# Kernel optimization log

Measured on AMD Instinct MI355X. Metric: run time of the kernel, lower is better.

The kernel has to match this reference:

```python
import jax, jax.numpy as jnp
import numpy as np

B, N, H = 32, 1024, 256
ALPHA = 0.2  # leaky relu slope
NEG_INF = -1e12


def setup_inputs() -> dict:
    key = jax.random.key(0)
    k1, k2, k3, k4, k5, k6 = jax.random.split(key, 6)
    inp = jax.random.normal(k1, (B, N, H), dtype=jnp.float32)
    A = (jax.random.uniform(k2, (B, N, N)) < 0.05).astype(jnp.float32)
    l = jnp.sort(jax.random.randint(k3, (B, 2), 0, N), axis=1)
    # xavier-uniform(gain=1.414) approximated; exact init values are irrelevant for correctness
    lim_w = 1.414 * np.sqrt(6.0 / (H + H))
    W_i = jax.random.uniform(k4, (H, H), minval=-lim_w, maxval=lim_w, dtype=jnp.float32)
    W_c = jax.random.uniform(k5, (H, H), minval=-lim_w, maxval=lim_w, dtype=jnp.float32)
    lim_a = 1.414 * np.sqrt(6.0 / (2 * H + 1))
    a = jax.random.uniform(k6, (2 * H, 1), minval=-lim_a, maxval=lim_a, dtype=jnp.float32)
    return {"inp": inp, "A": A, "l": l, "W_i": W_i, "W_c": W_c, "a": a}


def reference(inp, A, l, W_i, W_c, a):
    # eval mode: dropout is identity (training=False)
    n = inp.shape[1]
    h = inp.shape[2]
    Wh_i = jnp.einsum('bnh,he->bne', inp, W_i)
    Wh_c = jnp.einsum('bnh,he->bne', inp, W_c)
    # vectorized replacement of the per-batch Wh[index][i:j] = Wh_i[index][i:j] loop
    idx = jnp.arange(n)
    sel = (idx[None, :] >= l[:, 0:1]) & (idx[None, :] < l[:, 1:2])  # [B,N]
    Wh = jnp.where(sel[:, :, None], Wh_i, Wh_c)
    # additive attention scores
    Wh1 = Wh @ a[:h, :]  # [B,N,1]
    Wh2 = Wh @ a[h:, :]  # [B,N,1]
    A_ = A + jnp.eye(n, dtype=A.dtype)
    e = jax.nn.leaky_relu((Wh1 + jnp.swapaxes(Wh2, 1, 2)) * A_, ALPHA)
    att = jnp.where(A_ > 0, e, NEG_INF)
    att = jax.nn.softmax(att, axis=2)
    h_prime = jnp.einsum('bnm,bme->bne', att, Wh)
    return jax.nn.elu(h_prime)  # concat=True
```

## Files before the change

kernel.cpp:

```cpp
#include <hip/hip_runtime.h>
#include <hip/hip_bf16.h>
#include <stdint.h>

#define B_ 32
#define N_ 1024
#define H_ 256
#define PF_PITCH 520
#define GEMM_BLOCKS (B_ * 16)

typedef short bf16x8 __attribute__((ext_vector_type(8)));
typedef float floatx4 __attribute__((ext_vector_type(4)));

__device__ inline unsigned short f2bs(float x) {
    __hip_bfloat16 h = __float2bfloat16(x);
    return __builtin_bit_cast(unsigned short, h);
}

__global__ __launch_bounds__(256)
void k_pre(const float* __restrict__ Wi, const float* __restrict__ Wc,
           const float* __restrict__ a, float* __restrict__ U,
           unsigned short* __restrict__ WtFi, unsigned short* __restrict__ WtFc) {
    int bid = blockIdx.x;
    int t = threadIdx.x;
    if (bid < 32) {
        __shared__ float tile[64][65];
        int mat = bid >> 4;
        int tr = ((bid >> 2) & 3) * 64;
        int tc = (bid & 3) * 64;
        const float* W = mat ? Wc : Wi;
        unsigned short* WtF = mat ? WtFc : WtFi;
        int rr = t >> 2, c4 = (t & 3) * 16;
        const float* src = W + (size_t)(tr + rr) * H_ + tc + c4;
#pragma unroll
        for (int j = 0; j < 4; ++j) {
            float4 v = *reinterpret_cast<const float4*>(src + j * 4);
            tile[rr][c4 + 4 * j + 0] = v.x;
            tile[rr][c4 + 4 * j + 1] = v.y;
            tile[rr][c4 + 4 * j + 2] = v.z;
            tile[rr][c4 + 4 * j + 3] = v.w;
        }
        __syncthreads();
#pragma unroll
        for (int h = 0; h < 2; ++h) {
            int s = h * 256 + t;
            int ksl = s >> 8;
            int cl  = (s >> 6) & 3;
            int ll  = s & 63;
            int m16v = ll & 15, quadv = ll >> 4;
            int nloc = cl * 16 + m16v;
            int kb = ksl * 32 + quadv * 8;
            unsigned int pk[4];
#pragma unroll
            for (int jj = 0; jj < 4; ++jj) {
                unsigned short lo = f2bs(tile[kb + 2 * jj][nloc]);
                unsigned short hi = f2bs(tile[kb + 2 * jj + 1][nloc]);
                pk[jj] = (unsigned int)lo | ((unsigned int)hi << 16);
            }
            int ksg = (tr >> 5) + ksl;
            int cg  = (tc >> 4) + cl;
            *reinterpret_cast<uint4*>(WtF + ((size_t)(ksg * 16 + cg) * 64 + ll) * 8) =
                *reinterpret_cast<uint4*>(pk);
        }
    } else {
        int k = bid - 32;
        float wi = Wi[k * H_ + t];
        float wc = Wc[k * H_ + t];
        float a1 = a[t], a2 = a[H_ + t];
        float p0 = wi * a1, p1 = wc * a1, p2 = wi * a2, p3 = wc * a2;
        for (int off = 32; off; off >>= 1) {
            p0 += __shfl_xor(p0, off);
            p1 += __shfl_xor(p1, off);
            p2 += __shfl_xor(p2, off);
            p3 += __shfl_xor(p3, off);
        }
        __shared__ float red[4][4];
        int w = t >> 6;
        if ((t & 63) == 0) { red[w][0] = p0; red[w][1] = p1; red[w][2] = p2; red[w][3] = p3; }
        __syncthreads();
        if (t == 0) {
            U[0 * H_ + k] = red[0][0] + red[1][0] + red[2][0] + red[3][0];
            U[1 * H_ + k] = red[0][1] + red[1][1] + red[2][1] + red[3][1];
            U[2 * H_ + k] = red[0][2] + red[1][2] + red[2][2] + red[3][2];
            U[3 * H_ + k] = red[0][3] + red[1][3] + red[2][3] + red[3][3];
        }
    }
}

__global__ __launch_bounds__(256, 2)
void k_main(const float* __restrict__ inp, const int* __restrict__ l,
            const unsigned short* __restrict__ WtFi, const unsigned short* __restrict__ WtFc,
            unsigned short* __restrict__ WhF, const float* __restrict__ U,
            float* __restrict__ Wh1, float* __restrict__ Wh2,
            const float* __restrict__ A, unsigned int* __restrict__ M) {
    int bid = blockIdx.x;
    int t = threadIdx.x;
    int w = t >> 6;
    int lane = t & 63;
    if (bid >= GEMM_BLOCKS) {
        size_t row = bid - GEMM_BLOCKS;
        const float* Ar = A + row * N_ + w * 256 + lane * 4;
        float4 v = *reinterpret_cast<const float4*>(Ar);
        unsigned long long b0 = __ballot(v.x > 0.f);
        unsigned long long b1 = __ballot(v.y > 0.f);
        unsigned long long b2 = __ballot(v.z > 0.f);
        unsigned long long b3 = __ballot(v.w > 0.f);
        if (lane == 0) {
            unsigned int* Mp = M + (row * 4 + w) * 8;
            uint4 v0 = {(unsigned int)b0, (unsigned int)(b0 >> 32),
                        (unsigned int)b1, (unsigned int)(b1 >> 32)};
            uint4 v1 = {(unsigned int)b2, (unsigned int)(b2 >> 32),
                        (unsigned int)b3, (unsigned int)(b3 >> 32)};
            *reinterpret_cast<uint4*>(Mp) = v0;
            *reinterpret_cast<uint4*>(Mp + 4) = v1;
        }
        return;
    }

    __shared__ unsigned short bbuf[2][8192];
    int blk = bid;
    int b  = blk >> 4;
    int r0 = (blk & 15) * 64;
    int quad = lane >> 4, m16 = lane & 15;
    int rowb = r0 + w * 16;

    int l0 = l[2 * b], l1 = l[2 * b + 1];
    bool allI = (l0 <= r0) && (r0 + 64 <= l1);
    bool allC = (l1 <= r0) || (l0 >= r0 + 64);
    int npass = (allI || allC) ? 1 : 2;

    int row = rowb + m16;
    bool sel = (row >= l0) && (row < l1);
    const float* xrow = inp + ((size_t)(b * N_ + row)) * H_;
    const float* u1 = U + (sel ? 0 : H_);
    const float* u2 = U + 2 * H_ + (sel ? 0 : H_);

    float d1 = 0.f, d2 = 0.f;
#pragma unroll 2
    for (int ks = 0; ks < 8; ++ks) {
        const float4 xa = *reinterpret_cast<const float4*>(xrow + ks * 32 + quad * 8);
        const float4 xb = *reinterpret_cast<const float4*>(xrow + ks * 32 + quad * 8 + 4);
        const float4 ua = *reinterpret_cast<const float4*>(u1 + ks * 32 + quad * 8);
        const float4 ub = *reinterpret_cast<const float4*>(u1 + ks * 32 + quad * 8 + 4);
        const float4 va = *reinterpret_cast<const float4*>(u2 + ks * 32 + quad * 8);
        const float4 vb = *reinterpret_cast<const float4*>(u2 + ks * 32 + quad * 8 + 4);
        d1 += xa.x * ua.x + xa.y * ua.y + xa.z * ua.z + xa.w * ua.w
            + xb.x * ub.x + xb.y * ub.y + xb.z * ub.z + xb.w * ub.w;
        d2 += xa.x * va.x + xa.y * va.y + xa.z * va.z + xa.w * va.w
            + xb.x * vb.x + xb.y * vb.y + xb.z * vb.z + xb.w * vb.w;
    }
    d1 += __shfl_xor(d1, 16); d1 += __shfl_xor(d1, 32);
    d2 += __shfl_xor(d2, 16); d2 += __shfl_xor(d2, 32);
    if (quad == 0) {
        Wh1[b * N_ + rowb + m16] = d1;
        Wh2[b * N_ + rowb + m16] = d2;
    }

    unsigned short* fb = WhF + (size_t)b * (N_ * H_);
    int j0 = rowb + quad * 4;
    int ksO = j0 >> 5;
    int laneF = m16 + 16 * ((j0 & 31) >> 3);
    int jj0 = j0 & 7;

    for (int pass = 0; pass < npass; ++pass) {
        const unsigned short* gbase =
            (npass == 1) ? (allI ? WtFi : WtFc) : (pass == 0 ? WtFi : WtFc);

        floatx4 acc[16];
#pragma unroll
        for (int c = 0; c < 16; ++c) acc[c] = (floatx4){0.f, 0.f, 0.f, 0.f};

        {
            const unsigned short* s0 = gbase + (size_t)t * 32;
#pragma unroll
            for (int j = 0; j < 4; ++j)
                *reinterpret_cast<uint4*>(&bbuf[0][t * 32 + j * 8]) =
                    *reinterpret_cast<const uint4*>(s0 + j * 8);
        }
        for (int ks = 0; ks < 8; ++ks) {
            __syncthreads();
            uint4 v[4];
            if (ks < 7) {
                const unsigned short* sn = gbase + (size_t)(ks + 1) * 8192 + t * 32;
#pragma unroll
                for (int j = 0; j < 4; ++j)
                    v[j] = *reinterpret_cast<const uint4*>(sn + j * 8);
            }
            const float4 xa = *reinterpret_cast<const float4*>(xrow + ks * 32 + quad * 8);
            const float4 xb = *reinterpret_cast<const float4*>(xrow + ks * 32 + quad * 8 + 4);
            unsigned int pk0 = (unsigned int)f2bs(xa.x) | ((unsigned int)f2bs(xa.y) << 16);
            unsigned int pk1 = (unsigned int)f2bs(xa.z) | ((unsigned int)f2bs(xa.w) << 16);
            unsigned int pk2 = (unsigned int)f2bs(xb.x) | ((unsigned int)f2bs(xb.y) << 16);
            unsigned int pk3 = (unsigned int)f2bs(xb.z) | ((unsigned int)f2bs(xb.w) << 16);
            uint4 apk = {pk0, pk1, pk2, pk3};
            bf16x8 af = __builtin_bit_cast(bf16x8, apk);

            const unsigned short* bptr = &bbuf[ks & 1][lane * 8];
#pragma unroll
            for (int c = 0; c < 16; ++c) {
                bf16x8 bfr = *reinterpret_cast<const bf16x8*>(bptr + c * 512);
                acc[c] = __builtin_amdgcn_mfma_f32_16x16x32_bf16(af, bfr, acc[c], 0, 0, 0);
            }
            if (ks < 7) {
#pragma unroll
                for (int j = 0; j < 4; ++j)
                    *reinterpret_cast<uint4*>(&bbuf[(ks + 1) & 1][t * 32 + j * 8]) = v[j];
            }
        }
        __syncthreads();

#pragma unroll
        for (int c = 0; c < 16; ++c) {
            size_t base = ((size_t)((ksO * 16 + c) * 64) + laneF) * 8 + jj0;
            if (npass == 1) {
                unsigned int lo = (unsigned int)f2bs(acc[c][0]) | ((unsigned int)f2bs(acc[c][1]) << 16);
                unsigned int hi = (unsigned int)f2bs(acc[c][2]) | ((unsigned int)f2bs(acc[c][3]) << 16);
                uint2 v2 = {lo, hi};
                *reinterpret_cast<uint2*>(fb + base) = v2;
            } else {
                bool want[4]; bool all = true, none = true;
#pragma unroll
                for (int r = 0; r < 4; ++r) {
                    int j = j0 + r;
                    bool s2 = (j >= l0) && (j < l1);
                    want[r] = (pass == 0) ? s2 : !s2;
                    all = all && want[r]; none = none && !want[r];
                }
                if (all) {
                    unsigned int lo = (unsigned int)f2bs(acc[c][0]) | ((unsigned int)f2bs(acc[c][1]) << 16);
                    unsigned int hi = (unsigned int)f2bs(acc[c][2]) | ((unsigned int)f2bs(acc[c][3]) << 16);
                    uint2 v2 = {lo, hi};
                    *reinterpret_cast<uint2*>(fb + base) = v2;
                } else if (!none) {
#pragma unroll
                    for (int r = 0; r < 4; ++r)
                        if (want[r]) fb[base + r] = f2bs(acc[c][r]);
                }
            }
        }
    }
}

__global__ __launch_bounds__(256)
void k_attn(const unsigned int* __restrict__ Mask, const float* __restrict__ Wh1,
            const float* __restrict__ Wh2, const unsigned short* __restrict__ WhF,
            float* __restrict__ out) {
    __shared__ unsigned short pfrag[2][32 * PF_PITCH];
    __shared__ float rsum[2][16];
    int t = threadIdx.x, w = t >> 6, lane = t & 63;
    int bi = blockIdx.x;
    int b = (bi & 7) * 4 + (bi >> 8);
    int tile = (bi >> 3) & 31;
    int rowbase = tile * 32;

    const float* Wh2b = Wh2 + b * N_;
    float4 w2v[4];
#pragma unroll
    for (int ch = 0; ch < 4; ++ch)
        w2v[ch] = *reinterpret_cast<const float4*>(Wh2b + ch * 256 + lane * 4);

    int ksl = lane >> 3;
    int q2 = (lane >> 1) & 3;
    int jj0 = (lane & 1) * 4;
    int d  = lane >> 5;
    int lb = lane & 31;

#pragma unroll
    for (int tt = 0; tt < 2; ++tt) {
#pragma unroll
        for (int q = 0; q < 4; ++q) {
            int m = w * 4 + q;
            int i = rowbase + tt * 16 + m;
            float wh1 = Wh1[b * N_ + i];
            const uint2* Mrow = reinterpret_cast<const uint2*>(
                Mask + ((size_t)(b * N_ + i)) * 32);
            unsigned int wv[4][4];
#pragma unroll
            for (int ch = 0; ch < 4; ++ch)
#pragma unroll
                for (int c = 0; c < 4; ++c) {
                    uint2 u = Mrow[ch * 4 + c];
                    wv[ch][c] = d ? u.y : u.x;
                }
            int s = m + 16 * q2;
            int sw = s ^ ((s >> 3) & 7);
            int sls = sw * 8 + jj0;
            float rp = 0.f;
#pragma unroll
            for (int ch = 0; ch < 4; ++ch) {
                float aa[4];
#pragma unroll
                for (int c = 0; c < 4; ++c)
                    aa[c] = (float)((wv[ch][c] >> lb) & 1u);
                if ((i >> 2) == (ch * 64 + lane)) aa[i & 3] += 1.0f;
                float ww[4] = {w2v[ch].x, w2v[ch].y, w2v[ch].z, w2v[ch].w};
                float p[4];
#pragma unroll
                for (int c = 0; c < 4; ++c) {
                    float e  = (wh1 + ww[c]) * aa[c];
                    float lv = fmaxf(e, 0.2f * e);
                    p[c] = aa[c] > 0.f ? __expf(lv) : 0.f;
                }
                rp += (p[0] + p[1]) + (p[2] + p[3]);
                unsigned int lo = (unsigned int)f2bs(p[0]) | ((unsigned int)f2bs(p[1]) << 16);
                unsigned int hi = (unsigned int)f2bs(p[2]) | ((unsigned int)f2bs(p[3]) << 16);
                uint2 v = {lo, hi};
                int ks = ch * 8 + ksl;
                *reinterpret_cast<uint2*>(pfrag[tt] + ks * PF_PITCH + sls) = v;
            }
            for (int off = 32; off; off >>= 1) rp += __shfl_xor(rp, off);
            if (lane == 0) rsum[tt][m] = rp;
        }
    }
    __syncthreads();

    const unsigned short* WB = WhF + (size_t)b * (N_ * H_);
    int rs = (lane ^ ((lane >> 3) & 7)) * 8;
    floatx4 acc0[4], acc1[4];
#pragma unroll
    for (int cc = 0; cc < 4; ++cc) {
        acc0[cc] = (floatx4){0.f, 0.f, 0.f, 0.f};
        acc1[cc] = (floatx4){0.f, 0.f, 0.f, 0.f};
    }
    bf16x8 af0 = *reinterpret_cast<const bf16x8*>(pfrag[0] + rs);
    bf16x8 af1 = *reinterpret_cast<const bf16x8*>(pfrag[1] + rs);
    bf16x8 bfv[4];
#pragma unroll
    for (int cc = 0; cc < 4; ++cc)
        bfv[cc] = *reinterpret_cast<const bf16x8*>(
            WB + ((size_t)((w * 4 + cc) * 64 + lane)) * 8);
    for (int ks = 0; ks < 32; ++ks) {
        bf16x8 naf0, naf1, nbf[4];
        if (ks < 31) {
            naf0 = *reinterpret_cast<const bf16x8*>(pfrag[0] + (ks + 1) * PF_PITCH + rs);
            naf1 = *reinterpret_cast<const bf16x8*>(pfrag[1] + (ks + 1) * PF_PITCH + rs);
#pragma unroll
            for (int cc = 0; cc < 4; ++cc)
                nbf[cc] = *reinterpret_cast<const bf16x8*>(
                    WB + ((size_t)(((ks + 1) * 16 + w * 4 + cc) * 64 + lane)) * 8);
        }
#pragma unroll
        for (int cc = 0; cc < 4; ++cc) {
            acc0[cc] = __builtin_amdgcn_mfma_f32_16x16x32_bf16(af0, bfv[cc], acc0[cc], 0, 0, 0);
            acc1[cc] = __builtin_amdgcn_mfma_f32_16x16x32_bf16(af1, bfv[cc], acc1[cc], 0, 0, 0);
        }
        if (ks < 31) {
            af0 = naf0; af1 = naf1;
#pragma unroll
            for (int cc = 0; cc < 4; ++cc) bfv[cc] = nbf[cc];
        }
    }

    int quad = lane >> 4, m16 = lane & 15;
    float inv0[4], inv1[4];
#pragma unroll
    for (int r = 0; r < 4; ++r) {
        inv0[r] = 1.0f / rsum[0][quad * 4 + r];
        inv1[r] = 1.0f / rsum[1][quad * 4 + r];
    }
#pragma unroll
    for (int cc = 0; cc < 4; ++cc) {
        int col = (w * 4 + cc) * 16 + m16;
#pragma unroll
        for (int r = 0; r < 4; ++r) {
            int m = quad * 4 + r;
            float v0 = acc0[cc][r] * inv0[r];
            v0 = v0 > 0.f ? v0 : __expf(v0) - 1.0f;
            out[((size_t)(b * N_ + rowbase + m)) * H_ + col] = v0;
            float v1 = acc1[cc][r] * inv1[r];
            v1 = v1 > 0.f ? v1 : __expf(v1) - 1.0f;
            out[((size_t)(b * N_ + rowbase + 16 + m)) * H_ + col] = v1;
        }
    }
}

extern "C" void kernel_launch(void* const* d_in, const int* in_sizes, int n_in,
                              void* d_out, int out_size, void* d_ws, size_t ws_size,
                              hipStream_t stream) {
    const float* inp = (const float*)d_in[0];
    const float* A   = (const float*)d_in[1];
    const int*   l   = (const int*)d_in[2];
    const float* Wi  = (const float*)d_in[3];
    const float* Wc  = (const float*)d_in[4];
    const float* a   = (const float*)d_in[5];
    float* out = (float*)d_out;

    char* ws = (char*)d_ws;
    size_t off = 0;
    unsigned short* WhF  = (unsigned short*)(ws + off); off += (size_t)B_ * N_ * H_ * 2;
    float* Wh1 = (float*)(ws + off); off += (size_t)B_ * N_ * 4;
    float* Wh2 = (float*)(ws + off); off += (size_t)B_ * N_ * 4;
    float* U   = (float*)(ws + off); off += 4 * H_ * 4;
    unsigned short* WtFi = (unsigned short*)(ws + off); off += (size_t)H_ * H_ * 2;
    unsigned short* WtFc = (unsigned short*)(ws + off); off += (size_t)H_ * H_ * 2;
    unsigned int* Mask = (unsigned int*)(ws + off); off += (size_t)B_ * N_ * 32 * 4;

    k_pre<<<32 + H_, 256, 0, stream>>>(Wi, Wc, a, U, WtFi, WtFc);
    k_main<<<GEMM_BLOCKS + B_ * N_, 256, 0, stream>>>(inp, l, WtFi, WtFc, WhF, U,
                                                      Wh1, Wh2, A, Mask);
    k_attn<<<B_ * (N_ / 32), 256, 0, stream>>>(Mask, Wh1, Wh2, WhF, out);
}
```

Baseline: 310.2 us.

## Split adjacency bitmask into own kernel with multi-row blocks; coalesce weight tile loads

```diff
diff --git a/kernel.cpp b/kernel.cpp
--- a/kernel.cpp
+++ b/kernel.cpp
@@ -6,7 +6,6 @@
 #define N_ 1024
 #define H_ 256
 #define PF_PITCH 520
-#define GEMM_BLOCKS (B_ * 16)
 
 typedef short bf16x8 __attribute__((ext_vector_type(8)));
 typedef float floatx4 __attribute__((ext_vector_type(4)));
@@ -86,40 +85,50 @@
     }
 }
 
+__global__ __launch_bounds__(256)
+void k_abits(const float* __restrict__ A, unsigned int* __restrict__ M) {
+    int t = threadIdx.x, w = t >> 6, lane = t & 63;
+    int base = blockIdx.x * 16;
+#pragma unroll
+    for (int i0 = 0; i0 < 16; i0 += 4) {
+        float4 v[4];
+#pragma unroll
+        for (int k = 0; k < 4; ++k) {
+            size_t row = (size_t)(base + i0 + k);
+            v[k] = *reinterpret_cast<const float4*>(A + row * N_ + w * 256 + lane * 4);
+        }
+#pragma unroll
+        for (int k = 0; k < 4; ++k) {
+            size_t row = (size_t)(base + i0 + k);
+            unsigned long long b0 = __ballot(v[k].x > 0.f);
+            unsigned long long b1 = __ballot(v[k].y > 0.f);
+            unsigned long long b2 = __ballot(v[k].z > 0.f);
+            unsigned long long b3 = __ballot(v[k].w > 0.f);
+            if (lane == 0) {
+                unsigned int* Mp = M + (row * 4 + w) * 8;
+                uint4 v0 = {(unsigned int)b0, (unsigned int)(b0 >> 32),
+                            (unsigned int)b1, (unsigned int)(b1 >> 32)};
+                uint4 v1 = {(unsigned int)b2, (unsigned int)(b2 >> 32),
+                            (unsigned int)b3, (unsigned int)(b3 >> 32)};
+                *reinterpret_cast<uint4*>(Mp) = v0;
+                *reinterpret_cast<uint4*>(Mp + 4) = v1;
+            }
+        }
+    }
+}
+
 __global__ __launch_bounds__(256, 2)
-void k_main(const float* __restrict__ inp, const int* __restrict__ l,
+void k_gemm(const float* __restrict__ inp, const int* __restrict__ l,
             const unsigned short* __restrict__ WtFi, const unsigned short* __restrict__ WtFc,
             unsigned short* __restrict__ WhF, const float* __restrict__ U,
-            float* __restrict__ Wh1, float* __restrict__ Wh2,
-            const float* __restrict__ A, unsigned int* __restrict__ M) {
-    int bid = blockIdx.x;
+            float* __restrict__ Wh1, float* __restrict__ Wh2) {
+    __shared__ unsigned short bbuf[2][8192];
+    int blk = blockIdx.x;
+    int b  = blk >> 4;
+    int r0 = (blk & 15) * 64;
     int t = threadIdx.x;
     int w = t >> 6;
     int lane = t & 63;
-    if (bid >= GEMM_BLOCKS) {
-        size_t row = bid - GEMM_BLOCKS;
-        const float* Ar = A + row * N_ + w * 256 + lane * 4;
-        float4 v = *reinterpret_cast<const float4*>(Ar);
-        unsigned long long b0 = __ballot(v.x > 0.f);
-        unsigned long long b1 = __ballot(v.y > 0.f);
-        unsigned long long b2 = __ballot(v.z > 0.f);
-        unsigned long long b3 = __ballot(v.w > 0.f);
-        if (lane == 0) {
-            unsigned int* Mp = M + (row * 4 + w) * 8;
-            uint4 v0 = {(unsigned int)b0, (unsigned int)(b0 >> 32),
-                        (unsigned int)b1, (unsigned int)(b1 >> 32)};
-            uint4 v1 = {(unsigned int)b2, (unsigned int)(b2 >> 32),
-                        (unsigned int)b3, (unsigned int)(b3 >> 32)};
-            *reinterpret_cast<uint4*>(Mp) = v0;
-            *reinterpret_cast<uint4*>(Mp + 4) = v1;
-        }
-        return;
-    }
-
-    __shared__ unsigned short bbuf[2][8192];
-    int blk = bid;
-    int b  = blk >> 4;
-    int r0 = (blk & 15) * 64;
     int quad = lane >> 4, m16 = lane & 15;
     int rowb = r0 + w * 16;
 
@@ -170,20 +179,19 @@
         for (int c = 0; c < 16; ++c) acc[c] = (floatx4){0.f, 0.f, 0.f, 0.f};
 
         {
-            const unsigned short* s0 = gbase + (size_t)t * 32;
 #pragma unroll
             for (int j = 0; j < 4; ++j)
-                *reinterpret_cast<uint4*>(&bbuf[0][t * 32 + j * 8]) =
-                    *reinterpret_cast<const uint4*>(s0 + j * 8);
+                *reinterpret_cast<uint4*>(&bbuf[0][j * 2048 + t * 8]) =
+                    *reinterpret_cast<const uint4*>(gbase + j * 2048 + t * 8);
         }
         for (int ks = 0; ks < 8; ++ks) {
             __syncthreads();
             uint4 v[4];
             if (ks < 7) {
-                const unsigned short* sn = gbase + (size_t)(ks + 1) * 8192 + t * 32;
+                const unsigned short* sn = gbase + (size_t)(ks + 1) * 8192;
 #pragma unroll
                 for (int j = 0; j < 4; ++j)
-                    v[j] = *reinterpret_cast<const uint4*>(sn + j * 8);
+                    v[j] = *reinterpret_cast<const uint4*>(sn + j * 2048 + t * 8);
             }
             const float4 xa = *reinterpret_cast<const float4*>(xrow + ks * 32 + quad * 8);
             const float4 xb = *reinterpret_cast<const float4*>(xrow + ks * 32 + quad * 8 + 4);
@@ -203,7 +211,7 @@
             if (ks < 7) {
 #pragma unroll
                 for (int j = 0; j < 4; ++j)
-                    *reinterpret_cast<uint4*>(&bbuf[(ks + 1) & 1][t * 32 + j * 8]) = v[j];
+                    *reinterpret_cast<uint4*>(&bbuf[(ks + 1) & 1][j * 2048 + t * 8]) = v[j];
             }
         }
         __syncthreads();
@@ -395,7 +403,7 @@
     unsigned int* Mask = (unsigned int*)(ws + off); off += (size_t)B_ * N_ * 32 * 4;
 
     k_pre<<<32 + H_, 256, 0, stream>>>(Wi, Wc, a, U, WtFi, WtFc);
-    k_main<<<GEMM_BLOCKS + B_ * N_, 256, 0, stream>>>(inp, l, WtFi, WtFc, WhF, U,
-                                                      Wh1, Wh2, A, Mask);
+    k_abits<<<(B_ * N_) / 16, 256, 0, stream>>>(A, Mask);
+    k_gemm<<<B_ * 16, 256, 0, stream>>>(inp, l, WtFi, WtFc, WhF, U, Wh1, Wh2);
     k_attn<<<B_ * (N_ / 32), 256, 0, stream>>>(Mask, Wh1, Wh2, WhF, out);
 }
```

After: 299.8 us. 1.03x faster.
